# Kernel optimization log

Measured on AMD Instinct MI355X. Metric: run time of the kernel, lower is better.

Reference implementation:

```python
import jax, jax.numpy as jnp
import numpy as np
from jax import lax

G, N, S, K, R = 8, 4096, 2048, 64, 0.4   # graphs, nodes/graph, fps samples (ratio=0.5), max neighbors, radius
EPER = 65536                              # edges per graph (avg degree 16)
C = 13                                    # num_classes


def setup_inputs():
    key = jax.random.key(0)
    ks = jax.random.split(key, 8)
    norm = jax.random.normal(ks[0], (G * N, 3), jnp.float32)
    pos = jax.random.uniform(ks[1], (G * N, 3), jnp.float32)
    x = jax.random.normal(ks[2], (G * N, 2), jnp.float32)
    e = jax.random.randint(ks[3], (2, G, EPER), 0, N)
    off = (jnp.arange(G) * N)[None, :, None]
    edge_index = (e + off).reshape(2, G * EPER).astype(jnp.int64)
    batch = jnp.repeat(jnp.arange(G), N).astype(jnp.int64)
    def lin(k, i, o):
        return jax.random.normal(k, (i, o), jnp.float32) / np.float32(np.sqrt(i))
    W1 = lin(ks[4], 8, 64);    b1 = jnp.zeros((64,), jnp.float32)
    W2 = lin(ks[5], 72, 128);  b2 = jnp.zeros((128,), jnp.float32)
    W3 = lin(ks[6], 139, 256); b3 = jnp.zeros((256,), jnp.float32)
    lin_w = lin(ks[7], 256, C); lin_b = jnp.zeros((C,), jnp.float32)
    return dict(norm=norm, pos=pos, x=x, edge_index=edge_index, batch=batch,
                W1=W1, b1=b1, W2=W2, b2=b2, W3=W3, b3=b3, lin_w=lin_w, lin_b=lin_b)


def _gcn(h, src, dst, ew, W, b, n):
    # GCNConv(normalize=False): out[dst] += ew * (h @ W)[src]; + bias
    m = (h @ W)[src] * ew[:, None]
    return jax.ops.segment_sum(m, dst, num_segments=n) + b


def _fps(p):  # farthest point sampling on one graph, p: [N,3] -> [S] local indices (start at node 0)
    def step(carry, _):
        mind, cur = carry
        d = jnp.sum((p - p[cur]) ** 2, axis=1)
        mind = jnp.minimum(mind, d)
        return (mind, jnp.argmax(mind).astype(jnp.int32)), cur
    _, idx = lax.scan(step, (jnp.full((N,), jnp.inf, p.dtype), jnp.int32(0)), None, length=S)
    return idx


def _radius(p, q):  # p [N,3], q [S,3] -> neighbor cols [S,K] (lowest-index-first within radius), valid mask
    d2 = jnp.sum((q[:, None, :] - p[None, :, :]) ** 2, axis=-1)  # [S,N]
    mask = d2 < R * R
    score = jnp.where(mask, N - jnp.arange(N, dtype=jnp.int32)[None, :], 0)
    vals, cols = lax.top_k(score, K)
    valid = vals > 0
    return jnp.where(valid, cols, 0), valid


def reference(norm, pos, x, edge_index, batch, W1, b1, W2, b2, W3, b3, lin_w, lin_b):
    NT = G * N
    inp = jnp.concatenate([norm, pos, x], axis=1)          # [NT, 8]
    src, dst = edge_index[0], edge_index[1]
    ew = jnp.ones((src.shape[0],), inp.dtype)
    # dropout is inactive at inference (training=False)
    h1 = jax.nn.relu(_gcn(inp, src, dst, ew, W1, b1, NT))  # [NT, 64]
    h1 = jnp.concatenate([h1, inp], axis=1)                # [NT, 72]
    h2 = jax.nn.relu(_gcn(h1, src, dst, ew, W2, b2, NT))   # [NT, 128]

    pg = pos.reshape(G, N, 3)
    pgs = lax.stop_gradient(pg)
    idx_loc = jax.vmap(_fps)(pgs)                          # [G, S] local indices
    q = jax.vmap(lambda p, i: p[i])(pg, idx_loc)           # [G, S, 3] sampled positions
    cols, valid = jax.vmap(_radius)(pgs, lax.stop_gradient(q))  # [G, S, K]

    # PointConv with identity local_nn/global_nn: max over neighbors of [x_j, pos_j - pos_i]
    hg = h2.reshape(G, N, 128)
    def pconv(h, p, qv, c, v):
        msg = jnp.concatenate([h[c], p[c] - qv[:, None, :]], axis=-1)  # [S, K, 131]
        msg = jnp.where(v[..., None], msg, -jnp.inf)
        return jnp.max(msg, axis=1)                                    # [S, 131]
    x_int = jax.vmap(pconv)(hg, pg, q, cols, valid).reshape(G * S, 131)

    # filter_adj: keep edges with both endpoints sampled, remap to new ids
    idx_flat = (idx_loc + (jnp.arange(G) * N)[:, None]).reshape(-1)    # [G*S] global indices
    mapping = jnp.full((NT,), -1, jnp.int32).at[idx_flat].set(jnp.arange(G * S, dtype=jnp.int32))
    ns, nd = mapping[src], mapping[dst]
    em = (ns >= 0) & (nd >= 0)
    ew3 = em.astype(inp.dtype)
    ns = jnp.where(em, ns, 0)
    nd = jnp.where(em, nd, 0)

    h3in = jnp.concatenate([x_int, inp[idx_flat]], axis=1)  # [G*S, 139]
    h3 = jax.nn.relu(_gcn(h3in, ns, nd, ew3, W3, b3, G * S))  # [G*S, 256]

    pooled = h3.reshape(G, S, 256).max(axis=1)              # global_max_pool -> [G, 256]
    logits = pooled @ lin_w + lin_b
    out = jax.nn.log_softmax(logits, axis=1)
    pred = jax.nn.softmax(out, axis=1)
    return (out, pred)
```

## Files before the change

### kernel.cpp

```cpp
#include <hip/hip_runtime.h>
#include <hip/hip_bf16.h>

constexpr int NG   = 8;
constexpr int NPG  = 4096;
constexpr int NT   = NG * NPG;
constexpr int NS   = 2048;
constexpr int GS   = NG * NS;
constexpr int KN   = 64;
constexpr int NE   = NG * 65536;
constexpr int EPG  = 65536;
constexpr int NC   = 13;
constexpr int NWORK = 248;
constexpr int SPB  = 16;
constexpr int NF3B = GS / SPB;

__device__ __forceinline__ float inp_val(const float* norm, const float* pos, const float* x,
                                         int node, int dim) {
  if (dim < 3) return norm[(size_t)node * 3 + dim];
  if (dim < 6) return pos[(size_t)node * 3 + (dim - 3)];
  return x[(size_t)node * 2 + (dim - 6)];
}

__device__ __forceinline__ void wbar(int* ctrs, int k, int target) {
  __syncthreads();
  __threadfence();
  if (threadIdx.x == 0) {
    __hip_atomic_fetch_add(&ctrs[k], 1, __ATOMIC_RELEASE, __HIP_MEMORY_SCOPE_AGENT);
    while (__hip_atomic_load(&ctrs[k], __ATOMIC_ACQUIRE, __HIP_MEMORY_SCOPE_AGENT) < target)
      __builtin_amdgcn_s_sleep(16);
  }
  __syncthreads();
}

__global__ __launch_bounds__(256, 1) void phaseA_kernel(
    const float* __restrict__ pos, int* __restrict__ idxf, float* __restrict__ qpos,
    const float* __restrict__ norm, const float* __restrict__ x,
    const float* __restrict__ W1, float* __restrict__ t1,
    const int* __restrict__ ei, int* __restrict__ deg,
    int* __restrict__ off1, int* __restrict__ cur1, int* __restrict__ el1,
    const float* __restrict__ b1, const float* __restrict__ W2, float* __restrict__ t2,
    const float* __restrict__ b2, float* __restrict__ h2,
    int* __restrict__ wctr) {
  if (blockIdx.x >= 8) {
    const int wb = blockIdx.x - 8;
    const int sub = threadIdx.x >> 6;
    const int f = threadIdx.x & 63;
    __shared__ float wrow[4][80];
    __shared__ int sscan[256];
    for (int n0 = wb * 4; n0 < NT; n0 += NWORK * 4) {
      int n = n0 + sub;
      if (f < 8) wrow[sub][f] = inp_val(norm, pos, x, n, f);
      float acc = 0.f;
#pragma unroll
      for (int i = 0; i < 8; ++i) acc += wrow[sub][i] * W1[i * 64 + f];
      t1[(size_t)n * 64 + f] = acc;
    }
    for (int e = wb * 256 + threadIdx.x; e < NE; e += NWORK * 256)
      atomicAdd(&deg[ei[NE + e]], 1);
    wbar(wctr, 0, NWORK);
    if (wb == 0) {
      int t = threadIdx.x, base = t * 128, s = 0;
      for (int i = 0; i < 128; ++i) s += deg[base + i];
      sscan[t] = s;
      __syncthreads();
      for (int d = 1; d < 256; d <<= 1) {
        int v = (t >= d) ? sscan[t - d] : 0;
        __syncthreads();
        sscan[t] += v;
        __syncthreads();
      }
      int excl = (t == 0) ? 0 : sscan[t - 1];
      for (int i = 0; i < 128; ++i) { off1[base + i] = excl; excl += deg[base + i]; }
      if (t == 255) off1[NT] = sscan[255];
    }
    wbar(wctr, 1, NWORK);
    for (int e = wb * 256 + threadIdx.x; e < NE; e += NWORK * 256) {
      int sN = ei[e], dN = ei[NE + e];
      int p = off1[dN] + atomicAdd(&cur1[dN], 1);
      el1[p] = sN;
    }
    wbar(wctr, 2, NWORK);
    for (int n0 = wb * 4; n0 < NT; n0 += NWORK * 4) {
      int n = n0 + sub;
      int e0 = off1[n], e1 = off1[n + 1];
      float acc = 0.f;
      for (int j = e0; j < e1; ++j) acc += t1[(size_t)el1[j] * 64 + f];
      wrow[sub][f] = fmaxf(acc + b1[f], 0.f);
      if (f < 8) wrow[sub][64 + f] = inp_val(norm, pos, x, n, f);
      float a0 = 0.f, a1 = 0.f;
#pragma unroll 8
      for (int i = 0; i < 72; ++i) {
        float r = wrow[sub][i];
        a0 += r * W2[i * 128 + f];
        a1 += r * W2[i * 128 + 64 + f];
      }
      t2[(size_t)n * 128 + f] = a0;
      t2[(size_t)n * 128 + 64 + f] = a1;
    }
    wbar(wctr, 3, NWORK);
    {
      const int f2 = threadIdx.x & 127, sub2 = threadIdx.x >> 7;
      for (int n0 = wb * 2; n0 < NT; n0 += NWORK * 2) {
        int n = n0 + sub2;
        int e0 = off1[n], e1 = off1[n + 1];
        float acc = 0.f;
        for (int j = e0; j < e1; ++j) acc += t2[(size_t)el1[j] * 128 + f2];
        h2[(size_t)n * 128 + f2] = fmaxf(acc + b2[f2], 0.f);
      }
    }
    return;
  }
  const int g = blockIdx.x;
  __shared__ float4 sq[2][4];
  __shared__ int sidx[2][4];
  __shared__ float4 qrec[NS];
  __shared__ int irec[NS];
  const float* pg = pos + (size_t)g * NPG * 3;
  const int tid = threadIdx.x;
  const int wave = tid >> 6, lane = tid & 63;
  const int p0 = tid * 16;

  float a[48];
  {
    const float4* pg4 = reinterpret_cast<const float4*>(pg + (size_t)p0 * 3);
#pragma unroll
    for (int j = 0; j < 12; ++j) {
      float4 t = pg4[j];
      a[4 * j + 0] = t.x; a[4 * j + 1] = t.y; a[4 * j + 2] = t.z; a[4 * j + 3] = t.w;
    }
  }
  float px[16], py[16], pz[16], mind[16];
#pragma unroll
  for (int i = 0; i < 16; ++i) {
    px[i] = a[3 * i]; py[i] = a[3 * i + 1]; pz[i] = a[3 * i + 2];
    mind[i] = __int_as_float(0x7f800000);
  }
  float cx = pg[0], cy = pg[1], cz = pg[2];
  int idx_sel = 0;

  for (int s = 0; s < NS; ++s) {
    if (tid == 0) { irec[s] = idx_sel; qrec[s] = make_float4(cx, cy, cz, 0.f); }
    float bestv = -1.f, bx = 0.f, by = 0.f, bz = 0.f;
    int bi = 0;
#pragma unroll
    for (int i = 0; i < 16; ++i) {
      float dx = __fsub_rn(px[i], cx);
      float dy = __fsub_rn(py[i], cy);
      float dz = __fsub_rn(pz[i], cz);
      float dd = __fadd_rn(__fadd_rn(__fmul_rn(dx, dx), __fmul_rn(dy, dy)), __fmul_rn(dz, dz));
      float nm = fminf(mind[i], dd);
      mind[i] = nm;
      bool gt = nm > bestv;
      bestv = gt ? nm : bestv;
      bx = gt ? px[i] : bx;
      by = gt ? py[i] : by;
      bz = gt ? pz[i] : bz;
      bi = gt ? i : bi;
    }
    float v = bestv;
    v = fmaxf(v, __int_as_float(__builtin_amdgcn_update_dpp(0, __float_as_int(v), 0x111, 0xF, 0xF, true)));
    v = fmaxf(v, __int_as_float(__builtin_amdgcn_update_dpp(0, __float_as_int(v), 0x112, 0xF, 0xF, true)));
    v = fmaxf(v, __int_as_float(__builtin_amdgcn_update_dpp(0, __float_as_int(v), 0x114, 0xF, 0xF, true)));
    v = fmaxf(v, __int_as_float(__builtin_amdgcn_update_dpp(0, __float_as_int(v), 0x118, 0xF, 0xF, true)));
    v = fmaxf(v, __int_as_float(__builtin_amdgcn_update_dpp(0, __float_as_int(v), 0x142, 0xF, 0xF, true)));
    v = fmaxf(v, __int_as_float(__builtin_amdgcn_update_dpp(0, __float_as_int(v), 0x143, 0xF, 0xF, true)));
    int maxbits = __builtin_amdgcn_readlane(__float_as_int(v), 63);
    float wavemax = __int_as_float(maxbits);
    unsigned long long ball = __ballot(bestv == wavemax);
    int winner = __ffsll(ball) - 1;
    int b = s & 1;
    if (lane == winner) {
      sq[b][wave] = make_float4(bx, by, bz, wavemax);
      sidx[b][wave] = p0 + bi;
    }
    __syncthreads();
    float4 q0 = sq[b][0], q1 = sq[b][1], q2 = sq[b][2], q3 = sq[b][3];
    float4 qs = q3;
    if (q2.w >= qs.w) qs = q2;
    if (q1.w >= qs.w) qs = q1;
    if (q0.w >= qs.w) qs = q0;
    cx = qs.x; cy = qs.y; cz = qs.z;
    if (tid == 0) {
      int i0 = sidx[b][0], i1 = sidx[b][1], i2 = sidx[b][2], i3 = sidx[b][3];
      float r = q3.w; int is = i3;
      if (q2.w >= r) { r = q2.w; is = i2; }
      if (q1.w >= r) { r = q1.w; is = i1; }
      if (q0.w >= r) { r = q0.w; is = i0; }
      idx_sel = is;
    }
  }
  __syncthreads();
  for (int j = tid; j < NS; j += 256) {
    idxf[g * NS + j] = g * NPG + irec[j];
    float4 q = qrec[j];
    size_t m = (size_t)(g * NS + j) * 3;
    qpos[m + 0] = q.x; qpos[m + 1] = q.y; qpos[m + 2] = q.z;
  }
}

__global__ __launch_bounds__(256, 1) void radius_kernel(
    const float* __restrict__ pos, const float* __restrict__ qpos,
    int* __restrict__ cols, int* __restrict__ cnt,
    const int* __restrict__ idxf, int* __restrict__ mp) {
  __shared__ float spx[NPG], spy[NPG], spz[NPG];
  __shared__ int sbuf[KN][64][4];
  const int g = blockIdx.x & 7;
  const int s0 = (blockIdx.x >> 3) * 64;
  const float* pgc = pos + (size_t)g * NPG * 3;
  for (int i = threadIdx.x; i < NPG * 3; i += 256) {
    float v = pgc[i]; int node = i / 3, cc = i - node * 3;
    if (cc == 0) spx[node] = v; else if (cc == 1) spy[node] = v; else spz[node] = v;
  }
  __syncthreads();
  const int group = threadIdx.x >> 2;
  const int j = threadIdx.x & 3;
  const int m = g * NS + s0 + group;
  if (j == 0) mp[idxf[m]] = m;
  const float qx = qpos[(size_t)m * 3], qy = qpos[(size_t)m * 3 + 1],
              qz = qpos[(size_t)m * 3 + 2];
  int c = 0;
  const int i0 = j * 1024;
  for (int i = i0; i < i0 + 1024; ++i) {
    float dx = __fsub_rn(spx[i], qx);
    float dy = __fsub_rn(spy[i], qy);
    float dz = __fsub_rn(spz[i], qz);
    float d2 = __fadd_rn(__fadd_rn(__fmul_rn(dx, dx), __fmul_rn(dy, dy)), __fmul_rn(dz, dz));
    if (d2 < 0.16f) {
      sbuf[c][group][j] = i;
      if (++c == KN) break;
    }
  }
  const int lbase = (threadIdx.x & 63) & ~3;
  int c0 = __shfl(c, lbase + 0), c1 = __shfl(c, lbase + 1),
      c2 = __shfl(c, lbase + 2), c3 = __shfl(c, lbase + 3);
  int pre = (j > 0 ? c0 : 0) + (j > 1 ? c1 : 0) + (j > 2 ? c2 : 0);
  int total = c0 + c1 + c2 + c3;
  if (j == 0) cnt[m] = total < KN ? total : KN;
  int take = KN - pre;
  take = take < 0 ? 0 : (take > c ? c : take);
  int* outp = cols + (size_t)m * KN + pre;
  for (int i = 0; i < take; ++i) outp[i] = sbuf[i][group][j];
}

__global__ __launch_bounds__(256) void pointconv_kernel(const float* __restrict__ h2,
                                                        const float* __restrict__ pos,
                                                        const float* __restrict__ qpos,
                                                        const int* __restrict__ cols,
                                                        const int* __restrict__ cnt,
                                                        float* __restrict__ xint) {
  const int g = blockIdx.x & 7;
  const int chunk = blockIdx.x >> 3;
  const int ss = threadIdx.x >> 6;
  const int t = threadIdx.x & 63;
  const int m = g * NS + chunk * 4 + ss;
  int n = cnt[m];
  const int* cl = cols + (size_t)m * KN;
  float m0 = -INFINITY, m1 = -INFINITY, mp = -INFINITY;
  for (int k = 0; k < n; ++k) {
    int c = cl[k];
    size_t base = (size_t)(g * NPG + c);
    m0 = fmaxf(m0, h2[base * 128 + t]);
    m1 = fmaxf(m1, h2[base * 128 + 64 + t]);
    if (t < 3) mp = fmaxf(mp, pos[base * 3 + t]);
  }
  float* xo = xint + (size_t)m * 131;
  xo[t] = m0;
  xo[64 + t] = m1;
  if (t < 3) xo[128 + t] = __fsub_rn(mp, qpos[(size_t)m * 3 + t]);
}

__global__ void post2_kernel(const float* __restrict__ xint, const int* __restrict__ idxf,
                             const float* __restrict__ norm, const float* __restrict__ pos,
                             const float* __restrict__ x, const float* __restrict__ W3,
                             float* __restrict__ t3,
                             const int* __restrict__ ei, const int* __restrict__ mp,
                             int* __restrict__ deg) {
  if (blockIdx.x >= NF3B) {
    int wb = blockIdx.x - NF3B;
    int eb = (wb & 7) * 256 + (wb >> 3);
    int e = eb * 256 + threadIdx.x;
    int ns = mp[ei[e]], nd = mp[ei[NE + e]];
    if (ns >= 0 && nd >= 0) atomicAdd(&deg[nd], 1);
    return;
  }
  __shared__ float srow[SPB][140];
  const int m0 = blockIdx.x * SPB;
  for (int jj = threadIdx.x; jj < SPB * 139; jj += 256) {
    int sub = jj / 139, i = jj - sub * 139;
    int m = m0 + sub;
    srow[sub][i] = (i < 131) ? xint[(size_t)m * 131 + i]
                             : inp_val(norm, pos, x, idxf[m], i - 131);
  }
  __syncthreads();
  int f = threadIdx.x;
  float acc[SPB];
#pragma unroll
  for (int s = 0; s < SPB; ++s) acc[s] = 0.f;
#pragma unroll 4
  for (int i = 0; i < 139; ++i) {
    float wv = W3[i * 256 + f];
#pragma unroll
    for (int s = 0; s < SPB; ++s) acc[s] += srow[s][i] * wv;
  }
#pragma unroll
  for (int s = 0; s < SPB; ++s) t3[(size_t)(m0 + s) * 256 + f] = acc[s];
}

__global__ void fill2_kernel(const int* __restrict__ ei, const int* __restrict__ mp,
                             const int* __restrict__ off, int* __restrict__ cur,
                             int* __restrict__ el) {
  int b = blockIdx.x;
  int eb = (b & 7) * 256 + (b >> 3);
  int e = eb * 256 + threadIdx.x;
  int ns = mp[ei[e]], nd = mp[ei[NE + e]];
  if (ns >= 0 && nd >= 0) {
    int p = off[nd] + atomicAdd(&cur[nd], 1);
    el[p] = ns;
  }
}

__global__ __launch_bounds__(1024) void scan_kernel(const int* __restrict__ in,
                                                    int* __restrict__ out, int n) {
  __shared__ int ls[1024];
  int tid = threadIdx.x;
  int per = (n + 1023) >> 10;
  int base = tid * per;
  int s = 0;
  for (int i = 0; i < per; ++i) { int idx = base + i; if (idx < n) s += in[idx]; }
  ls[tid] = s;
  __syncthreads();
  for (int d = 1; d < 1024; d <<= 1) {
    int v = (tid >= d) ? ls[tid - d] : 0;
    __syncthreads();
    ls[tid] += v;
    __syncthreads();
  }
  int excl = (tid == 0) ? 0 : ls[tid - 1];
  for (int i = 0; i < per; ++i) {
    int idx = base + i;
    if (idx < n) { out[idx] = excl; excl += in[idx]; }
  }
  if (tid == 1023) out[n] = ls[1023];
}

__global__ void aggpool_kernel(const float* __restrict__ t, const int* __restrict__ off,
                               const int* __restrict__ el, const float* __restrict__ b,
                               float* __restrict__ pooled) {
  int node = (blockIdx.x & 7) * 2048 + (blockIdx.x >> 3);
  int f = threadIdx.x;
  int e0 = off[node], e1 = off[node + 1];
  float acc = 0.f;
  for (int j = e0; j < e1; ++j) acc += t[(size_t)el[j] * 256 + f];
  float val = fmaxf(acc + b[f], 0.f);
  atomicMax((int*)pooled + (node >> 11) * 256 + f, __float_as_int(val));
}

__global__ void head_kernel(const float* __restrict__ pooled, const float* __restrict__ lw,
                            const float* __restrict__ lb, float* __restrict__ outp) {
  __shared__ float lg[NG * NC];
  int t = threadIdx.x;
  if (t < NG * NC) {
    int g = t / NC, c = t % NC;
    float acc = lb[c];
    for (int k = 0; k < 256; ++k) acc += pooled[g * 256 + k] * lw[k * NC + c];
    lg[t] = acc;
  }
  __syncthreads();
  if (t < NG) {
    int g = t;
    float mx = -INFINITY;
    for (int c = 0; c < NC; ++c) mx = fmaxf(mx, lg[g * NC + c]);
    float sum = 0.f;
    for (int c = 0; c < NC; ++c) sum += expf(lg[g * NC + c] - mx);
    float lse = logf(sum);
    float ov[NC];
    float mx2 = -INFINITY;
    for (int c = 0; c < NC; ++c) {
      ov[c] = lg[g * NC + c] - mx - lse;
      outp[g * NC + c] = ov[c];
      mx2 = fmaxf(mx2, ov[c]);
    }
    float s2 = 0.f;
    for (int c = 0; c < NC; ++c) s2 += expf(ov[c] - mx2);
    for (int c = 0; c < NC; ++c) outp[NG * NC + g * NC + c] = expf(ov[c] - mx2) / s2;
  }
}

extern "C" void kernel_launch(void* const* d_in, const int* in_sizes, int n_in,
                              void* d_out, int out_size, void* d_ws, size_t ws_size,
                              hipStream_t stream) {
  const float* norm = (const float*)d_in[0];
  const float* pos  = (const float*)d_in[1];
  const float* x    = (const float*)d_in[2];
  const int* ei     = (const int*)d_in[3];
  const float* W1 = (const float*)d_in[5];
  const float* b1 = (const float*)d_in[6];
  const float* W2 = (const float*)d_in[7];
  const float* b2 = (const float*)d_in[8];
  const float* W3 = (const float*)d_in[9];
  const float* b3 = (const float*)d_in[10];
  const float* lw = (const float*)d_in[11];
  const float* lb = (const float*)d_in[12];
  float* outp = (float*)d_out;

  char* w = (char*)d_ws;
  size_t o = 0;
  auto alloc = [&](size_t bytes) -> void* {
    void* p = w + o;
    o = (o + bytes + 255) & ~(size_t)255;
    return p;
  };
  float* A    = (float*)alloc((size_t)NT * 128 * 4);
  float* Bf   = (float*)alloc((size_t)NT * 128 * 4);
  float* T1   = (float*)alloc((size_t)NT * 64 * 4);
  float* xint = (float*)alloc((size_t)GS * 131 * 4);
  int* cols   = (int*)alloc((size_t)GS * KN * 4);
  int* cnt    = (int*)alloc((size_t)GS * 4);
  int* deg1   = (int*)alloc((size_t)NT * 4);
  int* off1   = (int*)alloc((size_t)(NT + 1) * 4);
  int* cur1   = (int*)alloc((size_t)NT * 4);
  int* el1    = (int*)alloc((size_t)NE * 4);
  int* deg2   = (int*)alloc((size_t)GS * 4);
  int* off2   = (int*)alloc((size_t)(GS + 1) * 4);
  int* cur2   = (int*)alloc((size_t)GS * 4);
  int* el2    = (int*)alloc((size_t)NE * 4);
  int* idxf   = (int*)alloc((size_t)GS * 4);
  float* qpos = (float*)alloc((size_t)GS * 3 * 4);
  int* mapv   = (int*)alloc((size_t)NT * 4);
  float* pooled = (float*)alloc((size_t)NG * 256 * 4);
  int* wctr   = (int*)alloc(128);

  hipMemsetAsync(deg1, 0, (size_t)NT * 4, stream);
  hipMemsetAsync(cur1, 0, (size_t)NT * 4, stream);
  hipMemsetAsync(deg2, 0, (size_t)GS * 4, stream);
  hipMemsetAsync(cur2, 0, (size_t)GS * 4, stream);
  hipMemsetAsync(mapv, 0xFF, (size_t)NT * 4, stream);
  hipMemsetAsync(pooled, 0, (size_t)NG * 256 * 4, stream);
  hipMemsetAsync(wctr, 0, 128, stream);

  {
    void* ka[] = {(void*)&pos, (void*)&idxf, (void*)&qpos, (void*)&norm, (void*)&x,
                  (void*)&W1, (void*)&T1, (void*)&ei, (void*)&deg1,
                  (void*)&off1, (void*)&cur1, (void*)&el1,
                  (void*)&b1, (void*)&W2, (void*)&A, (void*)&b2, (void*)&Bf,
                  (void*)&wctr};
    hipLaunchCooperativeKernel((const void*)phaseA_kernel, dim3(8 + NWORK), dim3(256),
                               ka, 0, stream);
  }
  radius_kernel<<<256, 256, 0, stream>>>(pos, qpos, cols, cnt, idxf, mapv);
  pointconv_kernel<<<GS / 4, 256, 0, stream>>>(Bf, pos, qpos, cols, cnt, xint);
  post2_kernel<<<NF3B + NE / 256, 256, 0, stream>>>(xint, idxf, norm, pos, x, W3, A,
                                                    ei, mapv, deg2);
  scan_kernel<<<1, 1024, 0, stream>>>(deg2, off2, GS);
  fill2_kernel<<<NE / 256, 256, 0, stream>>>(ei, mapv, off2, cur2, el2);
  aggpool_kernel<<<GS, 256, 0, stream>>>(A, off2, el2, b3, pooled);
  head_kernel<<<1, 128, 0, stream>>>(pooled, lw, lb, outp);
}
```

Measured before the change: 1.996 ms.

## Pack two FPS graphs per block with flag sync and fuse pointconv into GCN3

The cooperative kernel moves to 512-thread blocks, and each FPS block now runs two graphs at once. That halves the FPS blocks from 8 to 4, leaving more worker blocks with wider strides. The per-step __syncthreads in FPS is replaced by per-wave sequence flags in LDS with a 4-slot ring, so each half-block synchronises independently. The pointconv max-gather is folded into the W3 transform kernel, which removes the xint round trip through global memory and one launch. The separate zeroing memsets are merged into one contiguous memset. The risks are register pressure at 512 threads, spin-wait cost, and the two FPS graphs competing for one CU's SIMDs on the serial critical path.

```diff
diff --git a/kernel.cpp b/kernel.cpp
--- a/kernel.cpp
+++ b/kernel.cpp
@@ -8,9 +8,8 @@
 constexpr int GS   = NG * NS;
 constexpr int KN   = 64;
 constexpr int NE   = NG * 65536;
-constexpr int EPG  = 65536;
 constexpr int NC   = 13;
-constexpr int NWORK = 248;
+constexpr int NWORK = 252;
 constexpr int SPB  = 16;
 constexpr int NF3B = GS / SPB;
 
@@ -32,7 +31,7 @@
   __syncthreads();
 }
 
-__global__ __launch_bounds__(256, 1) void phaseA_kernel(
+__global__ __launch_bounds__(512, 1) void phaseA_kernel(
     const float* __restrict__ pos, int* __restrict__ idxf, float* __restrict__ qpos,
     const float* __restrict__ norm, const float* __restrict__ x,
     const float* __restrict__ W1, float* __restrict__ t1,
@@ -41,56 +40,63 @@
     const float* __restrict__ b1, const float* __restrict__ W2, float* __restrict__ t2,
     const float* __restrict__ b2, float* __restrict__ h2,
     int* __restrict__ wctr) {
-  if (blockIdx.x >= 8) {
-    const int wb = blockIdx.x - 8;
-    const int sub = threadIdx.x >> 6;
+  if (blockIdx.x >= 4) {
+    const int wb = blockIdx.x - 4;
+    const int sub8 = threadIdx.x >> 6;
     const int f = threadIdx.x & 63;
-    __shared__ float wrow[4][80];
+    __shared__ float wrow[8][80];
     __shared__ int sscan[256];
-    for (int n0 = wb * 4; n0 < NT; n0 += NWORK * 4) {
-      int n = n0 + sub;
-      if (f < 8) wrow[sub][f] = inp_val(norm, pos, x, n, f);
+    for (int n0 = wb * 8; n0 < NT; n0 += NWORK * 8) {
+      int n = n0 + sub8;
+      if (f < 8) wrow[sub8][f] = inp_val(norm, pos, x, n, f);
       float acc = 0.f;
 #pragma unroll
-      for (int i = 0; i < 8; ++i) acc += wrow[sub][i] * W1[i * 64 + f];
+      for (int i = 0; i < 8; ++i) acc += wrow[sub8][i] * W1[i * 64 + f];
       t1[(size_t)n * 64 + f] = acc;
     }
-    for (int e = wb * 256 + threadIdx.x; e < NE; e += NWORK * 256)
+    for (int e = wb * 512 + threadIdx.x; e < NE; e += NWORK * 512)
       atomicAdd(&deg[ei[NE + e]], 1);
     wbar(wctr, 0, NWORK);
     if (wb == 0) {
-      int t = threadIdx.x, base = t * 128, s = 0;
-      for (int i = 0; i < 128; ++i) s += deg[base + i];
-      sscan[t] = s;
+      int t = threadIdx.x;
+      int s = 0;
+      if (t < 256) {
+        int base = t * 128;
+        for (int i = 0; i < 128; ++i) s += deg[base + i];
+        sscan[t] = s;
+      }
       __syncthreads();
       for (int d = 1; d < 256; d <<= 1) {
-        int v = (t >= d) ? sscan[t - d] : 0;
+        int v = (t < 256 && t >= d) ? sscan[t - d] : 0;
         __syncthreads();
-        sscan[t] += v;
+        if (t < 256) sscan[t] += v;
         __syncthreads();
       }
-      int excl = (t == 0) ? 0 : sscan[t - 1];
-      for (int i = 0; i < 128; ++i) { off1[base + i] = excl; excl += deg[base + i]; }
-      if (t == 255) off1[NT] = sscan[255];
+      if (t < 256) {
+        int base = t * 128;
+        int excl = (t == 0) ? 0 : sscan[t - 1];
+        for (int i = 0; i < 128; ++i) { off1[base + i] = excl; excl += deg[base + i]; }
+        if (t == 255) off1[NT] = sscan[255];
+      }
     }
     wbar(wctr, 1, NWORK);
-    for (int e = wb * 256 + threadIdx.x; e < NE; e += NWORK * 256) {
+    for (int e = wb * 512 + threadIdx.x; e < NE; e += NWORK * 512) {
       int sN = ei[e], dN = ei[NE + e];
       int p = off1[dN] + atomicAdd(&cur1[dN], 1);
       el1[p] = sN;
     }
     wbar(wctr, 2, NWORK);
-    for (int n0 = wb * 4; n0 < NT; n0 += NWORK * 4) {
-      int n = n0 + sub;
+    for (int n0 = wb * 8; n0 < NT; n0 += NWORK * 8) {
+      int n = n0 + sub8;
       int e0 = off1[n], e1 = off1[n + 1];
       float acc = 0.f;
       for (int j = e0; j < e1; ++j) acc += t1[(size_t)el1[j] * 64 + f];
-      wrow[sub][f] = fmaxf(acc + b1[f], 0.f);
-      if (f < 8) wrow[sub][64 + f] = inp_val(norm, pos, x, n, f);
+      wrow[sub8][f] = fmaxf(acc + b1[f], 0.f);
+      if (f < 8) wrow[sub8][64 + f] = inp_val(norm, pos, x, n, f);
       float a0 = 0.f, a1 = 0.f;
 #pragma unroll 8
       for (int i = 0; i < 72; ++i) {
-        float r = wrow[sub][i];
+        float r = wrow[sub8][i];
         a0 += r * W2[i * 128 + f];
         a1 += r * W2[i * 128 + 64 + f];
       }
@@ -100,7 +106,7 @@
     wbar(wctr, 3, NWORK);
     {
       const int f2 = threadIdx.x & 127, sub2 = threadIdx.x >> 7;
-      for (int n0 = wb * 2; n0 < NT; n0 += NWORK * 2) {
+      for (int n0 = wb * 4; n0 < NT; n0 += NWORK * 4) {
         int n = n0 + sub2;
         int e0 = off1[n], e1 = off1[n + 1];
         float acc = 0.f;
@@ -110,23 +116,29 @@
     }
     return;
   }
-  const int g = blockIdx.x;
-  __shared__ float4 sq[2][4];
-  __shared__ int sidx[2][4];
-  __shared__ float4 qrec[NS];
-  __shared__ int irec[NS];
+  __shared__ float4 qrec[2][NS];
+  __shared__ int irec[2][NS];
+  __shared__ float4 sqq[2][4][4];
+  __shared__ int sidq[2][4][4];
+  __shared__ unsigned seqq[2][4];
+  const int tid = threadIdx.x;
+  const int gsub = tid >> 8;
+  const int t = tid & 255;
+  const int w = (tid >> 6) & 3;
+  const int lane = tid & 63;
+  const int g = blockIdx.x * 2 + gsub;
+  const int p0 = t * 16;
+  if (tid < 8) seqq[tid >> 2][tid & 3] = 0u;
+  __syncthreads();
+
   const float* pg = pos + (size_t)g * NPG * 3;
-  const int tid = threadIdx.x;
-  const int wave = tid >> 6, lane = tid & 63;
-  const int p0 = tid * 16;
-
   float a[48];
   {
     const float4* pg4 = reinterpret_cast<const float4*>(pg + (size_t)p0 * 3);
 #pragma unroll
     for (int j = 0; j < 12; ++j) {
-      float4 t = pg4[j];
-      a[4 * j + 0] = t.x; a[4 * j + 1] = t.y; a[4 * j + 2] = t.z; a[4 * j + 3] = t.w;
+      float4 tt = pg4[j];
+      a[4 * j + 0] = tt.x; a[4 * j + 1] = tt.y; a[4 * j + 2] = tt.z; a[4 * j + 3] = tt.w;
     }
   }
   float px[16], py[16], pz[16], mind[16];
@@ -139,7 +151,7 @@
   int idx_sel = 0;
 
   for (int s = 0; s < NS; ++s) {
-    if (tid == 0) { irec[s] = idx_sel; qrec[s] = make_float4(cx, cy, cz, 0.f); }
+    if (t == 0) { irec[gsub][s] = idx_sel; qrec[gsub][s] = make_float4(cx, cy, cz, 0.f); }
     float bestv = -1.f, bx = 0.f, by = 0.f, bz = 0.f;
     int bi = 0;
 #pragma unroll
@@ -168,20 +180,34 @@
     float wavemax = __int_as_float(maxbits);
     unsigned long long ball = __ballot(bestv == wavemax);
     int winner = __ffsll(ball) - 1;
-    int b = s & 1;
+    const int slot = s & 3;
     if (lane == winner) {
-      sq[b][wave] = make_float4(bx, by, bz, wavemax);
-      sidx[b][wave] = p0 + bi;
-    }
-    __syncthreads();
-    float4 q0 = sq[b][0], q1 = sq[b][1], q2 = sq[b][2], q3 = sq[b][3];
+      sqq[gsub][slot][w] = make_float4(bx, by, bz, wavemax);
+      sidq[gsub][slot][w] = p0 + bi;
+    }
+    __threadfence_block();
+    if (lane == 0)
+      __hip_atomic_store(&seqq[gsub][w], (unsigned)(s + 1), __ATOMIC_RELEASE,
+                         __HIP_MEMORY_SCOPE_WORKGROUP);
+    const unsigned target = (unsigned)(s + 1);
+    for (;;) {
+      unsigned a0 = __hip_atomic_load(&seqq[gsub][0], __ATOMIC_ACQUIRE, __HIP_MEMORY_SCOPE_WORKGROUP);
+      unsigned a1 = __hip_atomic_load(&seqq[gsub][1], __ATOMIC_ACQUIRE, __HIP_MEMORY_SCOPE_WORKGROUP);
+      unsigned a2 = __hip_atomic_load(&seqq[gsub][2], __ATOMIC_ACQUIRE, __HIP_MEMORY_SCOPE_WORKGROUP);
+      unsigned a3 = __hip_atomic_load(&seqq[gsub][3], __ATOMIC_ACQUIRE, __HIP_MEMORY_SCOPE_WORKGROUP);
+      unsigned mn = min(min(a0, a1), min(a2, a3));
+      if (mn >= target) break;
+    }
+    float4 q0 = sqq[gsub][slot][0], q1 = sqq[gsub][slot][1];
+    float4 q2 = sqq[gsub][slot][2], q3 = sqq[gsub][slot][3];
     float4 qs = q3;
     if (q2.w >= qs.w) qs = q2;
     if (q1.w >= qs.w) qs = q1;
     if (q0.w >= qs.w) qs = q0;
     cx = qs.x; cy = qs.y; cz = qs.z;
-    if (tid == 0) {
-      int i0 = sidx[b][0], i1 = sidx[b][1], i2 = sidx[b][2], i3 = sidx[b][3];
+    if (t == 0) {
+      int i0 = sidq[gsub][slot][0], i1 = sidq[gsub][slot][1];
+      int i2 = sidq[gsub][slot][2], i3 = sidq[gsub][slot][3];
       float r = q3.w; int is = i3;
       if (q2.w >= r) { r = q2.w; is = i2; }
       if (q1.w >= r) { r = q1.w; is = i1; }
@@ -190,9 +216,9 @@
     }
   }
   __syncthreads();
-  for (int j = tid; j < NS; j += 256) {
-    idxf[g * NS + j] = g * NPG + irec[j];
-    float4 q = qrec[j];
+  for (int j = t; j < NS; j += 256) {
+    idxf[g * NS + j] = g * NPG + irec[gsub][j];
+    float4 q = qrec[gsub][j];
     size_t m = (size_t)(g * NS + j) * 3;
     qpos[m + 0] = q.x; qpos[m + 1] = q.y; qpos[m + 2] = q.z;
   }
@@ -242,39 +268,13 @@
   for (int i = 0; i < take; ++i) outp[i] = sbuf[i][group][j];
 }
 
-__global__ __launch_bounds__(256) void pointconv_kernel(const float* __restrict__ h2,
-                                                        const float* __restrict__ pos,
-                                                        const float* __restrict__ qpos,
-                                                        const int* __restrict__ cols,
-                                                        const int* __restrict__ cnt,
-                                                        float* __restrict__ xint) {
-  const int g = blockIdx.x & 7;
-  const int chunk = blockIdx.x >> 3;
-  const int ss = threadIdx.x >> 6;
-  const int t = threadIdx.x & 63;
-  const int m = g * NS + chunk * 4 + ss;
-  int n = cnt[m];
-  const int* cl = cols + (size_t)m * KN;
-  float m0 = -INFINITY, m1 = -INFINITY, mp = -INFINITY;
-  for (int k = 0; k < n; ++k) {
-    int c = cl[k];
-    size_t base = (size_t)(g * NPG + c);
-    m0 = fmaxf(m0, h2[base * 128 + t]);
-    m1 = fmaxf(m1, h2[base * 128 + 64 + t]);
-    if (t < 3) mp = fmaxf(mp, pos[base * 3 + t]);
-  }
-  float* xo = xint + (size_t)m * 131;
-  xo[t] = m0;
-  xo[64 + t] = m1;
-  if (t < 3) xo[128 + t] = __fsub_rn(mp, qpos[(size_t)m * 3 + t]);
-}
-
-__global__ void post2_kernel(const float* __restrict__ xint, const int* __restrict__ idxf,
-                             const float* __restrict__ norm, const float* __restrict__ pos,
-                             const float* __restrict__ x, const float* __restrict__ W3,
-                             float* __restrict__ t3,
-                             const int* __restrict__ ei, const int* __restrict__ mp,
-                             int* __restrict__ deg) {
+__global__ __launch_bounds__(256) void pcfeat3_kernel(
+    const float* __restrict__ h2, const float* __restrict__ pos,
+    const float* __restrict__ qpos, const int* __restrict__ cols,
+    const int* __restrict__ cnt, const int* __restrict__ idxf,
+    const float* __restrict__ norm, const float* __restrict__ x,
+    const float* __restrict__ W3, float* __restrict__ t3,
+    const int* __restrict__ ei, const int* __restrict__ mp, int* __restrict__ deg) {
   if (blockIdx.x >= NF3B) {
     int wb = blockIdx.x - NF3B;
     int eb = (wb & 7) * 256 + (wb >> 3);
@@ -284,12 +284,29 @@
     return;
   }
   __shared__ float srow[SPB][140];
-  const int m0 = blockIdx.x * SPB;
-  for (int jj = threadIdx.x; jj < SPB * 139; jj += 256) {
-    int sub = jj / 139, i = jj - sub * 139;
-    int m = m0 + sub;
-    srow[sub][i] = (i < 131) ? xint[(size_t)m * 131 + i]
-                             : inp_val(norm, pos, x, idxf[m], i - 131);
+  const int g = blockIdx.x & 7;
+  const int m0 = g * NS + (blockIdx.x >> 3) * SPB;
+  const int t = threadIdx.x & 63;
+  for (int it = 0; it < 4; ++it) {
+    int sl = it * 4 + (threadIdx.x >> 6);
+    int m = m0 + sl;
+    int n = cnt[m];
+    const int* cl = cols + (size_t)m * KN;
+    float v0 = -INFINITY, v1 = -INFINITY, mpv = -INFINITY;
+    for (int k = 0; k < n; ++k) {
+      int c = cl[k];
+      size_t base = (size_t)(g * NPG + c);
+      v0 = fmaxf(v0, h2[base * 128 + t]);
+      v1 = fmaxf(v1, h2[base * 128 + 64 + t]);
+      if (t < 3) mpv = fmaxf(mpv, pos[base * 3 + t]);
+    }
+    srow[sl][t] = v0;
+    srow[sl][64 + t] = v1;
+    if (t < 3) srow[sl][128 + t] = __fsub_rn(mpv, qpos[(size_t)m * 3 + t]);
+  }
+  for (int jj = threadIdx.x; jj < SPB * 8; jj += 256) {
+    int sl = jj >> 3, d = jj & 7;
+    srow[sl][131 + d] = inp_val(norm, pos, x, idxf[m0 + sl], d);
   }
   __syncthreads();
   int f = threadIdx.x;
@@ -410,33 +427,28 @@
     o = (o + bytes + 255) & ~(size_t)255;
     return p;
   };
+  int* deg1   = (int*)alloc((size_t)NT * 4);
+  int* cur1   = (int*)alloc((size_t)NT * 4);
+  int* deg2   = (int*)alloc((size_t)GS * 4);
+  int* cur2   = (int*)alloc((size_t)GS * 4);
+  float* pooled = (float*)alloc((size_t)NG * 256 * 4);
+  int* wctr   = (int*)alloc(128);
+  size_t zlen = o;
   float* A    = (float*)alloc((size_t)NT * 128 * 4);
   float* Bf   = (float*)alloc((size_t)NT * 128 * 4);
   float* T1   = (float*)alloc((size_t)NT * 64 * 4);
-  float* xint = (float*)alloc((size_t)GS * 131 * 4);
   int* cols   = (int*)alloc((size_t)GS * KN * 4);
   int* cnt    = (int*)alloc((size_t)GS * 4);
-  int* deg1   = (int*)alloc((size_t)NT * 4);
   int* off1   = (int*)alloc((size_t)(NT + 1) * 4);
-  int* cur1   = (int*)alloc((size_t)NT * 4);
   int* el1    = (int*)alloc((size_t)NE * 4);
-  int* deg2   = (int*)alloc((size_t)GS * 4);
   int* off2   = (int*)alloc((size_t)(GS + 1) * 4);
-  int* cur2   = (int*)alloc((size_t)GS * 4);
   int* el2    = (int*)alloc((size_t)NE * 4);
   int* idxf   = (int*)alloc((size_t)GS * 4);
   float* qpos = (float*)alloc((size_t)GS * 3 * 4);
   int* mapv   = (int*)alloc((size_t)NT * 4);
-  float* pooled = (float*)alloc((size_t)NG * 256 * 4);
-  int* wctr   = (int*)alloc(128);
-
-  hipMemsetAsync(deg1, 0, (size_t)NT * 4, stream);
-  hipMemsetAsync(cur1, 0, (size_t)NT * 4, stream);
-  hipMemsetAsync(deg2, 0, (size_t)GS * 4, stream);
-  hipMemsetAsync(cur2, 0, (size_t)GS * 4, stream);
+
+  hipMemsetAsync(w, 0, zlen, stream);
   hipMemsetAsync(mapv, 0xFF, (size_t)NT * 4, stream);
-  hipMemsetAsync(pooled, 0, (size_t)NG * 256 * 4, stream);
-  hipMemsetAsync(wctr, 0, 128, stream);
 
   {
     void* ka[] = {(void*)&pos, (void*)&idxf, (void*)&qpos, (void*)&norm, (void*)&x,
@@ -444,15 +456,14 @@
                   (void*)&off1, (void*)&cur1, (void*)&el1,
                   (void*)&b1, (void*)&W2, (void*)&A, (void*)&b2, (void*)&Bf,
                   (void*)&wctr};
-    hipLaunchCooperativeKernel((const void*)phaseA_kernel, dim3(8 + NWORK), dim3(256),
+    hipLaunchCooperativeKernel((const void*)phaseA_kernel, dim3(4 + NWORK), dim3(512),
                                ka, 0, stream);
   }
   radius_kernel<<<256, 256, 0, stream>>>(pos, qpos, cols, cnt, idxf, mapv);
-  pointconv_kernel<<<GS / 4, 256, 0, stream>>>(Bf, pos, qpos, cols, cnt, xint);
-  post2_kernel<<<NF3B + NE / 256, 256, 0, stream>>>(xint, idxf, norm, pos, x, W3, A,
-                                                    ei, mapv, deg2);
+  pcfeat3_kernel<<<NF3B + 2048, 256, 0, stream>>>(Bf, pos, qpos, cols, cnt, idxf,
+                                                  norm, x, W3, A, ei, mapv, deg2);
   scan_kernel<<<1, 1024, 0, stream>>>(deg2, off2, GS);
-  fill2_kernel<<<NE / 256, 256, 0, stream>>>(ei, mapv, off2, cur2, el2);
+  fill2_kernel<<<2048, 256, 0, stream>>>(ei, mapv, off2, cur2, el2);
   aggpool_kernel<<<GS, 256, 0, stream>>>(A, off2, el2, b3, pooled);
   head_kernel<<<1, 128, 0, stream>>>(pooled, lw, lb, outp);
 }
```

Result: slower. 2.704 ms (+35.5%).
